# Kernel tuning notes

Hardware: AMD Instinct MI355X
Metric: run time of the kernel (lower is better)

## Reference

```python
import jax, jax.numpy as jnp
import numpy as np
from jax import lax

SEQ, I, H = 8192, 512, 2048  # seq_len, input_size, hidden_size


def setup_inputs() -> dict:
    key = jax.random.key(0)
    ks = jax.random.split(key, 7)
    s_ih = 1.0 / np.sqrt(I)
    s_h = 1.0 / np.sqrt(H)
    return {
        "input": jax.random.normal(ks[0], (SEQ, I), dtype=jnp.float32),
        "W_ih": jax.random.normal(ks[1], (4 * H, I), dtype=jnp.float32) * s_ih,
        "W_hh": jax.random.normal(ks[2], (4 * H, H), dtype=jnp.float32) * s_h,
        "b_ih": jax.random.normal(ks[3], (4 * H,), dtype=jnp.float32) * s_h,
        "b_hh": jax.random.normal(ks[4], (4 * H,), dtype=jnp.float32) * s_h,
        "fc_w": jax.random.normal(ks[5], (1, H), dtype=jnp.float32) * s_h,
        "fc_b": jax.random.normal(ks[6], (1,), dtype=jnp.float32) * s_h,
    }


def reference(input, W_ih, W_hh, b_ih, b_hh, fc_w, fc_b):
    # Single-layer LSTM, batch=1, PyTorch gate order (i, f, g, o).
    b = b_ih + b_hh  # [4H]
    # Precompute input projections for all timesteps in one GEMM: [SEQ, 4H]
    x_proj = input @ W_ih.T + b
    h0 = jnp.zeros((H,), dtype=input.dtype)
    c0 = jnp.zeros((H,), dtype=input.dtype)

    def step(carry, xp_t):
        h, c = carry
        gates = xp_t + h @ W_hh.T  # [4H]
        i, f, g, o = jnp.split(gates, 4)
        c_new = jax.nn.sigmoid(f) * c + jax.nn.sigmoid(i) * jnp.tanh(g)
        h_new = jax.nn.sigmoid(o) * jnp.tanh(c_new)
        return (h_new, c_new), None

    (h_last, _), _ = lax.scan(step, (h0, c0), x_proj)
    # fc1 on last hidden state -> [1, 1]
    out = h_last @ fc_w.T + fc_b
    return out.reshape(1, 1)
```

## Files before the change

kernel.cpp:

```cpp
#include <hip/hip_runtime.h>
#include <hip/hip_bf16.h>

typedef _Float16 half2_t __attribute__((ext_vector_type(2)));
typedef _Float16 half8_t __attribute__((ext_vector_type(8)));
typedef float float4_t __attribute__((ext_vector_type(4)));

#define SEQ   8192
#define ISZ   512
#define HID   2048
#define G4H   8192
#define NB    256

#if __has_builtin(__builtin_amdgcn_fdot2)
#define DOT2(a, b, c) __builtin_amdgcn_fdot2((a), (b), (c), false)
#else
static __device__ __forceinline__ float DOT2(half2_t a, half2_t b, float c) {
    return c + (float)a.x * (float)b.x + (float)a.y * (float)b.y;
}
#endif

#if __has_builtin(__builtin_amdgcn_rcpf)
#define RCP(x) __builtin_amdgcn_rcpf(x)
#else
#define RCP(x) (1.0f / (x))
#endif

static __device__ __forceinline__ unsigned long long ld_u64(const void* p) {
    return __hip_atomic_load((const unsigned long long*)p, __ATOMIC_RELAXED,
                             __HIP_MEMORY_SCOPE_AGENT);
}
static __device__ __forceinline__ void st_u64(void* p, unsigned long long v) {
    __hip_atomic_store((unsigned long long*)p, v, __ATOMIC_RELAXED,
                       __HIP_MEMORY_SCOPE_AGENT);
}

template <int CTRL>
static __device__ __forceinline__ float dpp_add(float x) {
    int v = __builtin_amdgcn_update_dpp(0, __builtin_bit_cast(int, x), CTRL, 0xF,
                                        0xF, true);
    return x + __builtin_bit_cast(float, v);
}
#define DPP_XOR1  0xB1
#define DPP_XOR2  0x4E
#define DPP_XOR4  0x141
#define DPP_XOR8  0x128

__global__ __launch_bounds__(256) void cvt_f32_f16(const float* __restrict__ in,
                                                   _Float16* __restrict__ out, int n) {
    int i = (blockIdx.x * 256 + threadIdx.x) * 4;
    if (i < n) {
        float4 v = *(const float4*)(in + i);
        out[i + 0] = (_Float16)v.x;
        out[i + 1] = (_Float16)v.y;
        out[i + 2] = (_Float16)v.z;
        out[i + 3] = (_Float16)v.w;
    }
}

__global__ __launch_bounds__(256) void init_state(unsigned long long* __restrict__ words) {
    int i = blockIdx.x * 256 + threadIdx.x;
    if (i < 4096) words[i] = 0ull;
}

__global__ __launch_bounds__(256) void gemm_xproj(const _Float16* __restrict__ A,
                                                  const _Float16* __restrict__ B,
                                                  _Float16* __restrict__ C) {
    __shared__ _Float16 As[128 * 40];
    __shared__ _Float16 Bs[128 * 40];
    const int tid = threadIdx.x;
    const int bm = blockIdx.y, bn = blockIdx.x;
    const int wave = tid >> 6, lane = tid & 63;
    const int wr = wave >> 1, wc = wave & 1;
    const int l15 = lane & 15, lq = lane >> 4;

    float4_t acc[4][4];
#pragma unroll
    for (int im = 0; im < 4; im++)
#pragma unroll
        for (int in = 0; in < 4; in++)
#pragma unroll
            for (int r = 0; r < 4; r++) acc[im][in][r] = 0.f;

    for (int kt = 0; kt < ISZ; kt += 32) {
        __syncthreads();
#pragma unroll
        for (int ld = 0; ld < 2; ld++) {
            int c = tid + ld * 256;
            int r = c >> 2, ko = (c & 3) * 8;
            uint4 av = *(const uint4*)(A + (size_t)(bm * 128 + r) * ISZ + kt + ko);
            *(uint4*)(As + r * 40 + ko) = av;
            uint4 bv = *(const uint4*)(B + (size_t)(bn * 128 + r) * ISZ + kt + ko);
            *(uint4*)(Bs + r * 40 + ko) = bv;
        }
        __syncthreads();
        half8_t af[4], bf[4];
#pragma unroll
        for (int im = 0; im < 4; im++)
            af[im] = *(half8_t*)(As + (wr * 64 + im * 16 + l15) * 40 + lq * 8);
#pragma unroll
        for (int in = 0; in < 4; in++)
            bf[in] = *(half8_t*)(Bs + (wc * 64 + in * 16 + l15) * 40 + lq * 8);
#pragma unroll
        for (int im = 0; im < 4; im++)
#pragma unroll
            for (int in = 0; in < 4; in++)
                acc[im][in] = __builtin_amdgcn_mfma_f32_16x16x32_f16(af[im], bf[in], acc[im][in], 0, 0, 0);
    }
#pragma unroll
    for (int im = 0; im < 4; im++) {
        int mg = bm * 128 + wr * 64 + im * 16 + lq * 4;
#pragma unroll
        for (int in = 0; in < 4; in++) {
            int ng = bn * 128 + wc * 64 + in * 16 + l15;
            int gate = ng >> 11;
            int e = ng & 2047;
            int col2 = (e >> 3) * 32 + ((e >> 1) & 3) * 8 + gate * 2 + (e & 1);
#pragma unroll
            for (int r = 0; r < 4; r++)
                C[(size_t)(mg + r) * G4H + col2] = (_Float16)acc[im][in][r];
        }
    }
}

__global__ __launch_bounds__(256, 1) void lstm_persist(
    const float* __restrict__ Whh,
    const float* __restrict__ b_ih, const float* __restrict__ b_hh,
    const _Float16* __restrict__ xp,
    const float* __restrict__ fcw, const float* __restrict__ fcb,
    unsigned long long* __restrict__ words,
    float* __restrict__ out) {
    const int b = blockIdx.x, tid = threadIdx.x;
    const int g = tid >> 6, lane = tid & 63;
    const int pblk = (g << 6) | ((lane + b) & 63);

    __shared__ unsigned h_lds32[2][1280];

    half2_t w[8][16];
#pragma unroll
    for (int r = 0; r < 8; r++) {
        const float* wp =
            Whh + (size_t)((r >> 1) * HID + b * 8 + 2 * g + (r & 1)) * HID + lane * 32;
#pragma unroll
        for (int i = 0; i < 16; i++) {
            float2 f = *(const float2*)(wp + i * 2);
            half2_t h2;
            h2.x = (_Float16)f.x;
            h2.y = (_Float16)f.y;
            w[r][i] = h2;
        }
    }
    float bias_r = 0.f;
    if (lane < 8) {
        int row = ((lane >> 1) & 3) * HID + b * 8 + 2 * g + (lane & 1);
        bias_r = b_ih[row] + b_hh[row];
    }
    float c_reg = 0.f;

    const int s_dw = (pblk >> 2) * 20 + (pblk & 3) * 4;
    const int xpbase = b * 32 + g * 8;

    for (int t = 0; t < SEQ; ++t) {
        const unsigned ut = (unsigned)t;
        const int par = t & 1;

        float xpv = 0.f;
        if (lane < 8) xpv = (float)xp[(size_t)t * G4H + xpbase + lane];

        const unsigned long long* wp = words + (size_t)par * 2048 + pblk * 8;
        unsigned long long v0, v1, v2, v3;
        for (;;) {
            v0 = ld_u64(wp + 0);
            v1 = ld_u64(wp + 1);
            v2 = ld_u64(wp + 2);
            v3 = ld_u64(wp + 3);
            bool ok = ((unsigned)(v0 >> 32) >= ut) && ((unsigned)(v1 >> 32) >= ut) &&
                      ((unsigned)(v2 >> 32) >= ut) && ((unsigned)(v3 >> 32) >= ut);
            if (__all(ok)) break;
            __builtin_amdgcn_s_sleep(1);
        }

        *(uint4*)&h_lds32[par][s_dw] =
            make_uint4((unsigned)v0, (unsigned)v1, (unsigned)v2, (unsigned)v3);
        __syncthreads();

        union {
            uint4 q[4];
            half2_t h2[16];
        } hu;
        const uint4* hp4 = (const uint4*)((const char*)&h_lds32[par][0] + 80 * lane);
#pragma unroll
        for (int i = 0; i < 4; i++) hu.q[i] = hp4[i];

        float acc[8];
#pragma unroll
        for (int r = 0; r < 8; r++) {
            float a = 0.f;
#pragma unroll
            for (int i = 0; i < 16; i++) a = DOT2(w[r][i], hu.h2[i], a);
            acc[r] = a;
        }
#pragma unroll
        for (int r = 0; r < 8; r++) {
            acc[r] = dpp_add<DPP_XOR1>(acc[r]);
            acc[r] = dpp_add<DPP_XOR2>(acc[r]);
            acc[r] = dpp_add<DPP_XOR4>(acc[r]);
        }
        float u;
        {
            int s = lane & 7;
            float u01 = (s & 1) ? acc[1] : acc[0];
            float u23 = (s & 1) ? acc[3] : acc[2];
            float u45 = (s & 1) ? acc[5] : acc[4];
            float u67 = (s & 1) ? acc[7] : acc[6];
            float ua = (s & 2) ? u23 : u01;
            float ub = (s & 2) ? u67 : u45;
            u = (s & 4) ? ub : ua;
        }
        u = dpp_add<DPP_XOR8>(u);
        u += __shfl_xor(u, 16, 64);
        u += __shfl_xor(u, 32, 64);
        u += bias_r + xpv;

        {
            int base = lane & 1;
            float gi = __shfl(u, base + 0, 64);
            float gf = __shfl(u, base + 2, 64);
            float gg = __shfl(u, base + 4, 64);
            float go = __shfl(u, base + 6, 64);
            float si = RCP(1.f + __expf(-gi));
            float sf = RCP(1.f + __expf(-gf));
            float so = RCP(1.f + __expf(-go));
            float tg = 1.f - 2.f * RCP(1.f + __expf(2.f * gg));
            c_reg = sf * c_reg + si * tg;
            float tc = 1.f - 2.f * RCP(1.f + __expf(2.f * c_reg));
            float h = so * tc;
            _Float16 hf = (_Float16)h;
            unsigned pk = *(unsigned short*)&hf;
            unsigned pk1 = __shfl(pk, 1, 64);
            if (lane == 0) {
                unsigned lo = pk | (pk1 << 16);
                unsigned long long wword =
                    (unsigned long long)lo | ((unsigned long long)(ut + 1) << 32);
                st_u64(words + (size_t)((t + 1) & 1) * 2048 + b * 8 + g, wword);
            }
        }
    }

    if (b == 0) {
        const int par = SEQ & 1;
        const unsigned long long* wp = words + (size_t)par * 2048 + pblk * 8;
        unsigned long long v0, v1, v2, v3;
        for (;;) {
            v0 = ld_u64(wp + 0);
            v1 = ld_u64(wp + 1);
            v2 = ld_u64(wp + 2);
            v3 = ld_u64(wp + 3);
            bool ok = ((unsigned)(v0 >> 32) >= (unsigned)SEQ) &&
                      ((unsigned)(v1 >> 32) >= (unsigned)SEQ) &&
                      ((unsigned)(v2 >> 32) >= (unsigned)SEQ) &&
                      ((unsigned)(v3 >> 32) >= (unsigned)SEQ);
            if (__all(ok)) break;
            __builtin_amdgcn_s_sleep(1);
        }
        *(uint4*)&h_lds32[par][s_dw] =
            make_uint4((unsigned)v0, (unsigned)v1, (unsigned)v2, (unsigned)v3);
        __syncthreads();
        if (g == 0) {
            union {
                uint4 q[4];
                half2_t h2[16];
            } hu;
            const uint4* hp4 = (const uint4*)((const char*)&h_lds32[par][0] + 80 * lane);
#pragma unroll
            for (int i = 0; i < 4; i++) hu.q[i] = hp4[i];
            float s = 0.f;
            const float* fw = fcw + lane * 32;
#pragma unroll
            for (int i = 0; i < 16; i++)
                s += (float)hu.h2[i].x * fw[2 * i] + (float)hu.h2[i].y * fw[2 * i + 1];
#pragma unroll
            for (int off = 1; off < 64; off <<= 1) s += __shfl_xor(s, off, 64);
            if (lane == 0) out[0] = s + fcb[0];
        }
    }
}

extern "C" void kernel_launch(void* const* d_in, const int* in_sizes, int n_in,
                              void* d_out, int out_size, void* d_ws, size_t ws_size,
                              hipStream_t stream) {
    const float* input = (const float*)d_in[0];
    const float* W_ih = (const float*)d_in[1];
    const float* W_hh = (const float*)d_in[2];
    const float* b_ih = (const float*)d_in[3];
    const float* b_hh = (const float*)d_in[4];
    const float* fc_w = (const float*)d_in[5];
    const float* fc_b = (const float*)d_in[6];
    float* out = (float*)d_out;

    char* ws = (char*)d_ws;
    _Float16* xp16 = (_Float16*)ws;
    _Float16* A16 = (_Float16*)(ws + 134217728);
    _Float16* B16 = (_Float16*)(ws + 142606336);
    unsigned long long* words = (unsigned long long*)(ws + 134217728);

    cvt_f32_f16<<<(SEQ * ISZ) / 1024, 256, 0, stream>>>(input, A16, SEQ * ISZ);
    cvt_f32_f16<<<(G4H * ISZ) / 1024, 256, 0, stream>>>(W_ih, B16, G4H * ISZ);

    dim3 gg(G4H / 128, SEQ / 128);
    gemm_xproj<<<gg, 256, 0, stream>>>(A16, B16, xp16);

    init_state<<<16, 256, 0, stream>>>(words);

    lstm_persist<<<NB, 256, 0, stream>>>(W_hh, b_ih, b_hh, xp16, fc_w, fc_b,
                                         words, out);
}
```

Before: 15.05 ms.

## Halve persistent LSTM blocks to 128 with 512 threads each, prefetch next x_proj

Restructures the persistent recurrent kernel from 256 blocks of 256 threads to 128 blocks of 512 threads, so each block owns 16 hidden units and there are half as many grid-wide producers and consumers polling the step flags. The x_proj layout and the h exchange words are remapped to match, and each thread now polls two words instead of four. The next step's input projection is loaded one iteration ahead so its latency overlaps with the spin-wait. The aim is to cut per-step cross-block synchronisation cost, at the price of longer intra-block reductions and more pressure on one CU per block.

New measurement: 25.01 ms. 66.2% more time.

```diff
diff --git a/kernel.cpp b/kernel.cpp
--- a/kernel.cpp
+++ b/kernel.cpp
@@ -9,7 +9,8 @@
 #define ISZ   512
 #define HID   2048
 #define G4H   8192
-#define NB    256
+#define NB    128
+#define NT    512
 
 #if __has_builtin(__builtin_amdgcn_fdot2)
 #define DOT2(a, b, c) __builtin_amdgcn_fdot2((a), (b), (c), false)
@@ -44,6 +45,8 @@
 #define DPP_XOR2  0x4E
 #define DPP_XOR4  0x141
 #define DPP_XOR8  0x128
+
+#define TAGOK(v, t) ((unsigned)((v) >> 32) >= (t))
 
 __global__ __launch_bounds__(256) void cvt_f32_f16(const float* __restrict__ in,
                                                    _Float16* __restrict__ out, int n) {
@@ -59,7 +62,7 @@
 
 __global__ __launch_bounds__(256) void init_state(unsigned long long* __restrict__ words) {
     int i = blockIdx.x * 256 + threadIdx.x;
-    if (i < 4096) words[i] = 0ull;
+    if (i < 2048) words[i] = 0ull;
 }
 
 __global__ __launch_bounds__(256) void gemm_xproj(const _Float16* __restrict__ A,
@@ -114,7 +117,7 @@
             int ng = bn * 128 + wc * 64 + in * 16 + l15;
             int gate = ng >> 11;
             int e = ng & 2047;
-            int col2 = (e >> 3) * 32 + ((e >> 1) & 3) * 8 + gate * 2 + (e & 1);
+            int col2 = (e >> 4) * 64 + ((e >> 1) & 7) * 8 + gate * 2 + (e & 1);
 #pragma unroll
             for (int r = 0; r < 4; r++)
                 C[(size_t)(mg + r) * G4H + col2] = (_Float16)acc[im][in][r];
@@ -122,7 +125,7 @@
     }
 }
 
-__global__ __launch_bounds__(256, 1) void lstm_persist(
+__global__ __launch_bounds__(512, 1) void lstm_persist(
     const float* __restrict__ Whh,
     const float* __restrict__ b_ih, const float* __restrict__ b_hh,
     const _Float16* __restrict__ xp,
@@ -131,7 +134,8 @@
     float* __restrict__ out) {
     const int b = blockIdx.x, tid = threadIdx.x;
     const int g = tid >> 6, lane = tid & 63;
-    const int pblk = (g << 6) | ((lane + b) & 63);
+    const int sb = ((tid >> 2) + b) & 127;
+    const int k = tid & 3;
 
     __shared__ unsigned h_lds32[2][1280];
 
@@ -139,7 +143,7 @@
 #pragma unroll
     for (int r = 0; r < 8; r++) {
         const float* wp =
-            Whh + (size_t)((r >> 1) * HID + b * 8 + 2 * g + (r & 1)) * HID + lane * 32;
+            Whh + (size_t)((r >> 1) * HID + b * 16 + 2 * g + (r & 1)) * HID + lane * 32;
 #pragma unroll
         for (int i = 0; i < 16; i++) {
             float2 f = *(const float2*)(wp + i * 2);
@@ -151,36 +155,37 @@
     }
     float bias_r = 0.f;
     if (lane < 8) {
-        int row = ((lane >> 1) & 3) * HID + b * 8 + 2 * g + (lane & 1);
+        int row = ((lane >> 1) & 3) * HID + b * 16 + 2 * g + (lane & 1);
         bias_r = b_ih[row] + b_hh[row];
     }
     float c_reg = 0.f;
 
-    const int s_dw = (pblk >> 2) * 20 + (pblk & 3) * 4;
-    const int xpbase = b * 32 + g * 8;
+    const int s_dw = (sb >> 1) * 20 + 8 * (sb & 1) + 2 * k;
+    const int xpbase = b * 64 + g * 8;
+    const int pwid = sb * 8 + 2 * k;
+
+    float xpv_cur = 0.f;
+    if (lane < 8) xpv_cur = (float)xp[xpbase + lane];
 
     for (int t = 0; t < SEQ; ++t) {
         const unsigned ut = (unsigned)t;
         const int par = t & 1;
 
-        float xpv = 0.f;
-        if (lane < 8) xpv = (float)xp[(size_t)t * G4H + xpbase + lane];
-
-        const unsigned long long* wp = words + (size_t)par * 2048 + pblk * 8;
-        unsigned long long v0, v1, v2, v3;
+        float xpv_next = 0.f;
+        if (lane < 8 && t + 1 < SEQ)
+            xpv_next = (float)xp[(size_t)(t + 1) * G4H + xpbase + lane];
+        const float xpv = xpv_cur;
+
+        const unsigned long long* wp = words + (size_t)par * 1024 + pwid;
+        unsigned long long v0, v1;
         for (;;) {
             v0 = ld_u64(wp + 0);
             v1 = ld_u64(wp + 1);
-            v2 = ld_u64(wp + 2);
-            v3 = ld_u64(wp + 3);
-            bool ok = ((unsigned)(v0 >> 32) >= ut) && ((unsigned)(v1 >> 32) >= ut) &&
-                      ((unsigned)(v2 >> 32) >= ut) && ((unsigned)(v3 >> 32) >= ut);
-            if (__all(ok)) break;
+            if (__all(TAGOK(v0, ut) && TAGOK(v1, ut))) break;
             __builtin_amdgcn_s_sleep(1);
         }
 
-        *(uint4*)&h_lds32[par][s_dw] =
-            make_uint4((unsigned)v0, (unsigned)v1, (unsigned)v2, (unsigned)v3);
+        *(uint2*)&h_lds32[par][s_dw] = make_uint2((unsigned)v0, (unsigned)v1);
         __syncthreads();
 
         union {
@@ -241,29 +246,23 @@
                 unsigned lo = pk | (pk1 << 16);
                 unsigned long long wword =
                     (unsigned long long)lo | ((unsigned long long)(ut + 1) << 32);
-                st_u64(words + (size_t)((t + 1) & 1) * 2048 + b * 8 + g, wword);
+                st_u64(words + (size_t)((t + 1) & 1) * 1024 + b * 8 + g, wword);
             }
         }
+        xpv_cur = xpv_next;
     }
 
     if (b == 0) {
         const int par = SEQ & 1;
-        const unsigned long long* wp = words + (size_t)par * 2048 + pblk * 8;
-        unsigned long long v0, v1, v2, v3;
+        const unsigned long long* wp = words + (size_t)par * 1024 + pwid;
+        unsigned long long v0, v1;
         for (;;) {
             v0 = ld_u64(wp + 0);
             v1 = ld_u64(wp + 1);
-            v2 = ld_u64(wp + 2);
-            v3 = ld_u64(wp + 3);
-            bool ok = ((unsigned)(v0 >> 32) >= (unsigned)SEQ) &&
-                      ((unsigned)(v1 >> 32) >= (unsigned)SEQ) &&
-                      ((unsigned)(v2 >> 32) >= (unsigned)SEQ) &&
-                      ((unsigned)(v3 >> 32) >= (unsigned)SEQ);
-            if (__all(ok)) break;
+            if (__all(TAGOK(v0, (unsigned)SEQ) && TAGOK(v1, (unsigned)SEQ))) break;
             __builtin_amdgcn_s_sleep(1);
         }
-        *(uint4*)&h_lds32[par][s_dw] =
-            make_uint4((unsigned)v0, (unsigned)v1, (unsigned)v2, (unsigned)v3);
+        *(uint2*)&h_lds32[par][s_dw] = make_uint2((unsigned)v0, (unsigned)v1);
         __syncthreads();
         if (g == 0) {
             union {
@@ -309,8 +308,8 @@
     dim3 gg(G4H / 128, SEQ / 128);
     gemm_xproj<<<gg, 256, 0, stream>>>(A16, B16, xp16);
 
-    init_state<<<16, 256, 0, stream>>>(words);
-
-    lstm_persist<<<NB, 256, 0, stream>>>(W_hh, b_ih, b_hh, xp16, fc_w, fc_b,
-                                         words, out);
-}
+    init_state<<<8, 256, 0, stream>>>(words);
+
+    lstm_persist<<<NB, NT, 0, stream>>>(W_hh, b_ih, b_hh, xp16, fc_w, fc_b,
+                                        words, out);
+}
```
